# Performance work log

Hardware: AMD Instinct MI355X
Metric: run time of the kernel (lower is better)

## Reference

```python
import jax, jax.numpy as jnp
import numpy as np

IN_F, OUT_F, STRIPE = 2048, 8192, 256
NUM_STRIPES = OUT_F // STRIPE  # 32
B, S = 2, 1024


def setup_inputs() -> dict:
    key = jax.random.key(0)
    k = jax.random.split(key, 6)
    return {
        "x": jax.random.normal(k[0], (B, S, IN_F), dtype=jnp.float32),
        "weight": jax.random.normal(k[1], (IN_F, OUT_F), dtype=jnp.float32) / IN_F ** 0.5,
        "bias": jax.random.normal(k[2], (OUT_F,), dtype=jnp.float32) * 0.02,
        "mu": jax.random.normal(k[3], (IN_F,), dtype=jnp.float32) * 0.1,
        "std": jax.random.uniform(k[4], (IN_F,), dtype=jnp.float32, minval=0.5, maxval=1.5),
        "thresholds": jax.random.uniform(k[5], (NUM_STRIPES, IN_F), dtype=jnp.float32),
    }


def reference(x, weight, bias, mu, std, thresholds):
    # Inference (no-grad) path of CWICLinear.forward.
    og_shape = x.shape[:-1]
    I = x.shape[-1]
    O = weight.shape[1]
    ns = thresholds.shape[0]
    ss = O // ns

    xm = x.reshape(-1, 1, I) - mu[None, None, :]          # [N, 1, I]
    thr = (thresholds * std[None, :])[None]               # [1, ns, I]
    mask = (jnp.abs(xm) > thr).astype(x.dtype)            # [N, ns, I]
    xh = xm * mask                                        # [N, ns, I]

    Wr = weight.T.reshape(ns, ss, I)                      # [ns, ss, I]
    # per-stripe batched mat-vec: y[n, r, s] = sum_i xh[n, r, i] * Wr[r, s, i]
    y = jnp.einsum('nri,rsi->nrs', xh, Wr).reshape(-1, O)
    post_mu = mu @ weight                                 # einsum('ab,a->b')
    y = y + post_mu[None, :] + bias[None, :]

    dense_flops = jnp.full(og_shape, float(I * O), dtype=jnp.float32)
    sparse_flops = (float(I * O) * mask.mean(axis=(1, 2))).reshape(og_shape).astype(jnp.float32)
    return y.reshape(*og_shape, O), (dense_flops, sparse_flops)
```

## Files before the change

### kernel.cpp

```cpp
#include <hip/hip_runtime.h>
#include <hip/hip_bf16.h>
#include <stdint.h>

#define IN_F 2048
#define OUT_F 8192
#define NROWS 2048
#define NS 32

typedef float  vf4  __attribute__((ext_vector_type(4)));
typedef short  vs4  __attribute__((ext_vector_type(4)));
typedef short  vs8  __attribute__((ext_vector_type(8)));
typedef float  vacc __attribute__((ext_vector_type(4)));
typedef unsigned int vu4 __attribute__((ext_vector_type(4)));

__device__ __forceinline__ short f2bf(float f) {
    return __builtin_bit_cast(short, __float2bfloat16(f));
}

__device__ __forceinline__ void gl2lds16(const void* g, void* l) {
    __builtin_amdgcn_global_load_lds((__attribute__((address_space(1))) void*)g,
                                     (__attribute__((address_space(3))) void*)l,
                                     16, 0, 0);
}

__global__ void __launch_bounds__(256) k_thr(const float* __restrict__ thresholds,
                                             const float* __restrict__ stdv,
                                             float* __restrict__ thr,
                                             float* __restrict__ dense) {
    int gid = blockIdx.x * 256 + threadIdx.x;
    int idx = gid * 4;
    vf4 t = *(const vf4*)(thresholds + idx);
    vf4 s = *(const vf4*)(stdv + (idx & (IN_F - 1)));
    *(vf4*)(thr + idx) = t * s;
    if (gid < NROWS / 4) {
        vf4 d = {16777216.0f, 16777216.0f, 16777216.0f, 16777216.0f};
        *(vf4*)(dense + gid * 4) = d;
    }
}

__global__ void __launch_bounds__(256) k_wt(const float* __restrict__ W,
                                            char* __restrict__ Wt) {
    __shared__ float tile[64 * 64];
    __shared__ unsigned int tbf[64 * 33];
    int kt = blockIdx.x & 31;
    int ot = blockIdx.x >> 5;
    int t = threadIdx.x;
    int kbase = kt * 64, obase = ot * 64;
#pragma unroll
    for (int rr = 0; rr < 4; ++rr) {
        int r = rr * 16 + (t >> 4);
        int c = (t & 15) * 4;
        *(vf4*)(tile + r * 64 + c) =
            *(const vf4*)(W + (size_t)(kbase + r) * OUT_F + obase + c);
    }
    __syncthreads();
    int o = t & 63;
    int kc2 = (t >> 6) * 8;
#pragma unroll
    for (int j = 0; j < 8; ++j) {
        unsigned short lo = (unsigned short)f2bf(tile[(kc2 * 2 + 2 * j) * 64 + o]);
        unsigned short hi = (unsigned short)f2bf(tile[(kc2 * 2 + 2 * j + 1) * 64 + o]);
        tbf[o * 33 + kc2 + j] = (unsigned)lo | ((unsigned)hi << 16);
    }
    __syncthreads();
    int r = t >> 2, seg = t & 3;
    unsigned int d[8];
#pragma unroll
    for (int i = 0; i < 8; ++i) d[i] = tbf[r * 33 + seg * 8 + i];
    int s = (r & 7) << 4;
    char* rowp = Wt + (size_t)(obase + r) * 4096 + kt * 128;
    vu4 a = {d[0], d[1], d[2], d[3]};
    vu4 b = {d[4], d[5], d[6], d[7]};
    *(vu4*)(rowp + ((seg * 32) ^ s)) = a;
    *(vu4*)(rowp + ((seg * 32 + 16) ^ s)) = b;
}

#define LDS_A  0
#define LDS_B  16384

struct XR { vf4 a[8]; };

__global__ void __launch_bounds__(256, 2) k_gemm(const float* __restrict__ x,
                                                 const char* __restrict__ Wt,
                                                 const float* __restrict__ bias,
                                                 const float* __restrict__ mu,
                                                 const float* __restrict__ thr,
                                                 float* __restrict__ y,
                                                 float* __restrict__ sparse) {
    __shared__ char lds[49152];
    __shared__ int scnt[128];

    int bid = blockIdx.x;
    int xcd = bid & 7, idx = bid >> 3;
    int mt = (xcd >> 2) * 8 + (idx & 7);
    int nt = (xcd & 3) * 16 + (idx >> 3);
    int m_base = mt * 128, n_base = nt * 128;
    const float* thrR = thr + (size_t)(nt >> 1) * IN_F;

    int t = threadIdx.x;
    int w = t >> 6, lane = t & 63;
    int lane16 = lane & 15, g = lane >> 4;
    int wm = w >> 1, wn = w & 1;

    int col4 = lane16 * 4;
    const float* xbase = x + (size_t)(m_base + w * 32 + g) * IN_F + col4;

    int brow = lane >> 3, bcol = (lane & 7) * 16;

    auto stageB = [&](int kt, int buf) {
#pragma unroll
        for (int q = 0; q < 4; ++q) {
            const char* src = Wt + (size_t)(n_base + (w * 4 + q) * 8 + brow) * 4096 +
                              kt * 128 + bcol;
            gl2lds16(src, lds + LDS_B + buf * 16384 + (w * 4 + q) * 1024);
        }
    };
    auto load_x = [&](int kt, XR& r) {
        const float* p = xbase + kt * 64;
#pragma unroll
        for (int v = 0; v < 8; ++v)
            r.a[v] = *(const vf4*)(p + (size_t)v * 4 * IN_F);
    };

    vacc acc[4][4];
#pragma unroll
    for (int i = 0; i < 4; ++i)
#pragma unroll
        for (int j = 0; j < 4; ++j)
            acc[i][j] = (vacc){0.f, 0.f, 0.f, 0.f};
    int cnt[8] = {0, 0, 0, 0, 0, 0, 0, 0};

    XR xa, xb;
    stageB(0, 0);
    load_x(0, xa);

    auto xform = [&](XR& r, vf4 mv, vf4 tv) {
#pragma unroll
        for (int v = 0; v < 8; ++v) {
            vf4 xv = r.a[v];
            vs4 o;
#pragma unroll
            for (int j = 0; j < 4; ++j) {
                float xm = xv[j] - mv[j];
                bool m = __builtin_fabsf(xm) > tv[j];
                cnt[v] += m ? 1 : 0;
                o[j] = f2bf(m ? xv[j] : mv[j]);
            }
            int row = w * 32 + v * 4 + g;
            *(vs4*)(lds + LDS_A + row * 128 + ((lane16 * 8) ^ ((row & 7) << 4))) = o;
        }
    };

    auto compute = [&](int buf) {
        const char* bbase = lds + LDS_B + buf * 16384;
#pragma unroll
        for (int ks = 0; ks < 2; ++ks) {
            vs8 af[4], bf[4];
#pragma unroll
            for (int i = 0; i < 4; ++i) {
                int row = wm * 64 + i * 16 + lane16;
                af[i] = *(const vs8*)(lds + LDS_A + row * 128 +
                                      ((ks * 64 + g * 16) ^ ((row & 7) << 4)));
                int col = wn * 64 + i * 16 + lane16;
                bf[i] = *(const vs8*)(bbase + col * 128 +
                                      ((ks * 64 + g * 16) ^ ((col & 7) << 4)));
            }
#pragma unroll
            for (int i = 0; i < 4; ++i)
#pragma unroll
                for (int j = 0; j < 4; ++j)
                    acc[i][j] = __builtin_amdgcn_mfma_f32_16x16x32_bf16(
                        af[i], bf[j], acc[i][j], 0, 0, 0);
        }
    };

    auto step = [&](int kt, XR& cur, XR& nxt) {
        bool pre = kt < 31;
        vf4 mv = *(const vf4*)(mu + kt * 64 + col4);
        vf4 tv = *(const vf4*)(thrR + kt * 64 + col4);
        if (pre) load_x(kt + 1, nxt);
        __builtin_amdgcn_sched_barrier(0);
        __builtin_amdgcn_s_barrier();
        __builtin_amdgcn_sched_barrier(0);
        if (pre) stageB(kt + 1, (kt + 1) & 1);
        xform(cur, mv, tv);
        if (pre) asm volatile("s_waitcnt vmcnt(12)" ::: "memory");
        else     asm volatile("s_waitcnt vmcnt(0)" ::: "memory");
        asm volatile("s_waitcnt lgkmcnt(0)" ::: "memory");
        __builtin_amdgcn_s_barrier();
        __builtin_amdgcn_sched_barrier(0);
        compute(kt & 1);
    };

    for (int kt = 0; kt < 32; kt += 2) {
        step(kt, xa, xb);
        step(kt + 1, xb, xa);
    }

    float* yb = y + (size_t)(m_base + wm * 64) * OUT_F + n_base + wn * 64;
#pragma unroll
    for (int j = 0; j < 4; ++j) {
        int ng = j * 16 + lane16;
        float bv = bias[n_base + wn * 64 + ng];
#pragma unroll
        for (int i = 0; i < 4; ++i) {
            int mg = i * 16 + g * 4;
#pragma unroll
            for (int q = 0; q < 4; ++q)
                yb[(size_t)(mg + q) * OUT_F + ng] = acc[i][j][q] + bv;
        }
    }

    if (t < 128) scnt[t] = 0;
    __syncthreads();
    if ((nt & 1) == 0) {
#pragma unroll
        for (int v = 0; v < 8; ++v)
            atomicAdd(&scnt[w * 32 + v * 4 + g], cnt[v]);
        __syncthreads();
        if (t < 128)
            atomicAdd(sparse + m_base + t, 256.0f * (float)scnt[t]);
    }
}

extern "C" void kernel_launch(void* const* d_in, const int* in_sizes, int n_in,
                              void* d_out, int out_size, void* d_ws, size_t ws_size,
                              hipStream_t stream) {
    const float* x = (const float*)d_in[0];
    const float* W = (const float*)d_in[1];
    const float* bias = (const float*)d_in[2];
    const float* mu = (const float*)d_in[3];
    const float* stdv = (const float*)d_in[4];
    const float* thresholds = (const float*)d_in[5];

    float* y = (float*)d_out;
    float* dense = y + (size_t)NROWS * OUT_F;
    float* sparse = dense + NROWS;

    char* Wt = (char*)d_ws;
    float* thr = (float*)(Wt + (size_t)OUT_F * IN_F * 2);

    hipLaunchKernelGGL(k_thr, dim3((NS * IN_F) / 1024), dim3(256), 0, stream,
                       thresholds, stdv, thr, dense);
    hipLaunchKernelGGL(k_wt, dim3((IN_F / 64) * (OUT_F / 64)), dim3(256), 0, stream,
                       W, Wt);
    hipMemsetAsync(sparse, 0, NROWS * sizeof(float), stream);
    hipLaunchKernelGGL(k_gemm, dim3((NROWS / 128) * (OUT_F / 128)), dim3(256), 0,
                       stream, x, Wt, bias, mu, thr, y, sparse);
}
```

Before: 268.8 us.

## Double-buffer the A tile and overlap its transform with MFMA compute

The masked, bf16-converted x tile (A) now lives in two LDS buffers, and the B buffers move up to make room. Each k-step splits its MFMA work into two halves and places the transform for the next tile and the global loads for the tile after it between them, so only one barrier is needed per step instead of two. Loads for x, mu and the thresholds are prefetched two tiles ahead. LDS use grows to about 64.5 KB per block, and the per-row count scratch reuses the LDS array, which may limit occupancy under the launch bound of two blocks per CU. The extra registers held for the deeper prefetch also add pressure.

```diff
diff --git a/kernel.cpp b/kernel.cpp
--- a/kernel.cpp
+++ b/kernel.cpp
@@ -76,7 +76,7 @@
 }
 
 #define LDS_A  0
-#define LDS_B  16384
+#define LDS_B  32768
 
 struct XR { vf4 a[8]; };
 
@@ -87,8 +87,7 @@
                                                  const float* __restrict__ thr,
                                                  float* __restrict__ y,
                                                  float* __restrict__ sparse) {
-    __shared__ char lds[49152];
-    __shared__ int scnt[128];
+    __shared__ char lds[66048];
 
     int bid = blockIdx.x;
     int xcd = bid & 7, idx = bid >> 3;
@@ -130,11 +129,8 @@
             acc[i][j] = (vacc){0.f, 0.f, 0.f, 0.f};
     int cnt[8] = {0, 0, 0, 0, 0, 0, 0, 0};
 
-    XR xa, xb;
-    stageB(0, 0);
-    load_x(0, xa);
-
-    auto xform = [&](XR& r, vf4 mv, vf4 tv) {
+    auto xform = [&](XR& r, vf4 mv, vf4 tv, int abuf) {
+        char* abase = lds + LDS_A + abuf * 16384;
 #pragma unroll
         for (int v = 0; v < 8; ++v) {
             vf4 xv = r.a[v];
@@ -147,54 +143,77 @@
                 o[j] = f2bf(m ? xv[j] : mv[j]);
             }
             int row = w * 32 + v * 4 + g;
-            *(vs4*)(lds + LDS_A + row * 128 + ((lane16 * 8) ^ ((row & 7) << 4))) = o;
-        }
-    };
-
-    auto compute = [&](int buf) {
+            *(vs4*)(abase + row * 128 + ((lane16 * 8) ^ ((row & 7) << 4))) = o;
+        }
+    };
+
+    auto compute_ks = [&](int ks, int buf) {
+        const char* abase = lds + LDS_A + buf * 16384;
         const char* bbase = lds + LDS_B + buf * 16384;
-#pragma unroll
-        for (int ks = 0; ks < 2; ++ks) {
-            vs8 af[4], bf[4];
-#pragma unroll
-            for (int i = 0; i < 4; ++i) {
-                int row = wm * 64 + i * 16 + lane16;
-                af[i] = *(const vs8*)(lds + LDS_A + row * 128 +
-                                      ((ks * 64 + g * 16) ^ ((row & 7) << 4)));
-                int col = wn * 64 + i * 16 + lane16;
-                bf[i] = *(const vs8*)(bbase + col * 128 +
-                                      ((ks * 64 + g * 16) ^ ((col & 7) << 4)));
-            }
-#pragma unroll
-            for (int i = 0; i < 4; ++i)
-#pragma unroll
-                for (int j = 0; j < 4; ++j)
-                    acc[i][j] = __builtin_amdgcn_mfma_f32_16x16x32_bf16(
-                        af[i], bf[j], acc[i][j], 0, 0, 0);
-        }
-    };
-
-    auto step = [&](int kt, XR& cur, XR& nxt) {
-        bool pre = kt < 31;
-        vf4 mv = *(const vf4*)(mu + kt * 64 + col4);
-        vf4 tv = *(const vf4*)(thrR + kt * 64 + col4);
-        if (pre) load_x(kt + 1, nxt);
+        vs8 af[4], bf[4];
+#pragma unroll
+        for (int i = 0; i < 4; ++i) {
+            int row = wm * 64 + i * 16 + lane16;
+            af[i] = *(const vs8*)(abase + row * 128 +
+                                  ((ks * 64 + g * 16) ^ ((row & 7) << 4)));
+            int col = wn * 64 + i * 16 + lane16;
+            bf[i] = *(const vs8*)(bbase + col * 128 +
+                                  ((ks * 64 + g * 16) ^ ((col & 7) << 4)));
+        }
+#pragma unroll
+        for (int i = 0; i < 4; ++i)
+#pragma unroll
+            for (int j = 0; j < 4; ++j)
+                acc[i][j] = __builtin_amdgcn_mfma_f32_16x16x32_bf16(
+                    af[i], bf[j], acc[i][j], 0, 0, 0);
+    };
+
+    XR xa, xb;
+    vf4 m0, t0, m1, t1;
+
+    load_x(0, xa);
+    m0 = *(const vf4*)(mu + col4);
+    t0 = *(const vf4*)(thrR + col4);
+    stageB(0, 0);
+    __builtin_amdgcn_sched_barrier(0);
+    xform(xa, m0, t0, 0);
+    load_x(1, xb);
+    m1 = *(const vf4*)(mu + 64 + col4);
+    t1 = *(const vf4*)(thrR + 64 + col4);
+    __builtin_amdgcn_sched_barrier(0);
+    asm volatile("s_waitcnt vmcnt(10)" ::: "memory");
+    asm volatile("s_waitcnt lgkmcnt(0)" ::: "memory");
+    __builtin_amdgcn_sched_barrier(0);
+    __builtin_amdgcn_s_barrier();
+    __builtin_amdgcn_sched_barrier(0);
+
+    auto step = [&](int kt, XR& xcur, XR& xnxt, vf4& mvc, vf4& tvc,
+                    vf4& mvn, vf4& tvn) {
+        int cur = kt & 1, nxt = cur ^ 1;
+        if (kt < 31) stageB(kt + 1, nxt);
         __builtin_amdgcn_sched_barrier(0);
-        __builtin_amdgcn_s_barrier();
+        compute_ks(0, cur);
+        if (kt < 31) xform(xcur, mvc, tvc, nxt);
+        if (kt < 30) {
+            load_x(kt + 2, xnxt);
+            mvn = *(const vf4*)(mu + (kt + 2) * 64 + col4);
+            tvn = *(const vf4*)(thrR + (kt + 2) * 64 + col4);
+        }
         __builtin_amdgcn_sched_barrier(0);
-        if (pre) stageB(kt + 1, (kt + 1) & 1);
-        xform(cur, mv, tv);
-        if (pre) asm volatile("s_waitcnt vmcnt(12)" ::: "memory");
-        else     asm volatile("s_waitcnt vmcnt(0)" ::: "memory");
-        asm volatile("s_waitcnt lgkmcnt(0)" ::: "memory");
-        __builtin_amdgcn_s_barrier();
-        __builtin_amdgcn_sched_barrier(0);
-        compute(kt & 1);
+        compute_ks(1, cur);
+        if (kt < 30)      asm volatile("s_waitcnt vmcnt(10)" ::: "memory");
+        else if (kt < 31) asm volatile("s_waitcnt vmcnt(0)" ::: "memory");
+        if (kt < 31) {
+            asm volatile("s_waitcnt lgkmcnt(0)" ::: "memory");
+            __builtin_amdgcn_sched_barrier(0);
+            __builtin_amdgcn_s_barrier();
+            __builtin_amdgcn_sched_barrier(0);
+        }
     };
 
     for (int kt = 0; kt < 32; kt += 2) {
-        step(kt, xa, xb);
-        step(kt + 1, xb, xa);
+        step(kt, xb, xa, m1, t1, m0, t0);
+        step(kt + 1, xa, xb, m0, t0, m1, t1);
     }
 
     float* yb = y + (size_t)(m_base + wm * 64) * OUT_F + n_base + wn * 64;
@@ -211,6 +230,8 @@
         }
     }
 
+    int* scnt = (int*)lds;
+    __syncthreads();
     if (t < 128) scnt[t] = 0;
     __syncthreads();
     if ((nt & 1) == 0) {
```

New measurement: 241.0 us. 10.3% less time.
